# Kernel optimization log

Hardware: AMD Instinct MI355X
Metric: run time of the kernel (lower is better)

The kernel has to match this reference:

```python
import jax, jax.numpy as jnp
import numpy as np

B, N, C, H, PD, CLN = 8, 1024, 512, 8, 256, 64
HD = C // H
HID = 4 * C
LN_EPS = 1e-5
ATT_EPS = 1e-6


def layernorm(x, g, b):
    mu = x.mean(-1, keepdims=True)
    var = ((x - mu) ** 2).mean(-1, keepdims=True)
    return (x - mu) * jax.lax.rsqrt(var + LN_EPS) * g + b


def setup_inputs() -> dict:
    key = jax.random.key(0)
    ks = jax.random.split(key, 16)
    p = lambda k, shp, s=0.02: (jax.random.normal(k, shp, dtype=jnp.float32) * s)
    return {
        "x_token": jax.random.normal(ks[0], (B, N, C), dtype=jnp.float32),
        "x_path": jax.random.normal(ks[1], (B, N, PD), dtype=jnp.float32),
        "wq": p(ks[2], (C, C)),
        "wk": p(ks[3], (C, C)),
        "wv": p(ks[4], (C, C)),
        "w_proj": p(ks[5], (C, C)),
        "b_proj": jnp.zeros((C,), jnp.float32),
        "g1": jnp.ones((C,), jnp.float32),
        "b1": jnp.zeros((C,), jnp.float32),
        "g2": jnp.ones((C,), jnp.float32),
        "b2": jnp.zeros((C,), jnp.float32),
        "w1": p(ks[6], (HID, C)),
        "bb1": jnp.zeros((HID,), jnp.float32),
        "w2": p(ks[7], (C, HID)),
        "bb2": jnp.zeros((C,), jnp.float32),
        "idx_cluster": jax.random.randint(ks[8], (B, N), 0, CLN, dtype=jnp.int64 if jax.config.jax_enable_x64 else jnp.int32),
        "cluster_num": CLN,
    }


def reference(x_token, x_path, wq, wk, wv, w_proj, b_proj, g1, b1, g2, b2,
              w1, bb1, w2, bb2, idx_cluster, cluster_num):
    Bn, Nn, Cn = x_token.shape
    scale = (Cn // H) ** -0.5

    # norm1 + attention
    t = layernorm(x_token, g1, b1)
    q = (t @ wq.T).reshape(Bn, Nn, H, HD).transpose(0, 2, 1, 3)  # bhnd
    k = (t @ wk.T).reshape(Bn, Nn, H, HD).transpose(0, 2, 1, 3)
    v = (t @ wv.T).reshape(Bn, Nn, H, HD).transpose(0, 2, 1, 3)

    # scatter-to-(B,cluster,N,C) then sum over clusters == same-cluster mask on QK^T
    scores = jnp.einsum("bhid,bhjd->bhij", q, k) * scale  # (B,H,N,N)
    same = (idx_cluster[:, None, :, None] == idx_cluster[:, None, None, :])  # (B,1,N,N)
    scores = jnp.where(same, scores, jnp.float32(-1e9))

    # custom eps-stabilized exp-softmax (as in the torch code, no max-subtraction)
    e = jnp.exp(scores.astype(jnp.float32))
    attn = (e + ATT_EPS / Nn) / (e.sum(-1, keepdims=True) + ATT_EPS)

    out = jnp.einsum("bhij,bhjd->bhid", attn, v)
    out = out.transpose(0, 2, 1, 3).reshape(Bn, Nn, Cn)
    out = out @ w_proj.T + b_proj

    x = x_token + out  # drop_path is identity in eval

    # MLP block
    h = layernorm(x, g2, b2)
    m = jax.nn.gelu(h @ w1.T + bb1, approximate=False) @ w2.T + bb2
    return x + m
```

## Files before the change

kernel.cpp:

```cpp
#include <hip/hip_runtime.h>

typedef unsigned short u16;
typedef __attribute__((ext_vector_type(4))) float f32x4;
typedef __attribute__((ext_vector_type(8))) short s16x8;
typedef __attribute__((ext_vector_type(4))) unsigned short u16x4;
typedef __attribute__((ext_vector_type(8))) unsigned short u16x8;

__device__ __forceinline__ u16 f2bf(float f) {
    unsigned int u = __builtin_bit_cast(unsigned int, f);
    u += 0x7fffu + ((u >> 16) & 1u);
    return (u16)(u >> 16);
}
__device__ __forceinline__ float bf2f(u16 h) {
    unsigned int u = ((unsigned int)h) << 16;
    return __builtin_bit_cast(float, u);
}
__device__ __forceinline__ void gload16(const u16* g, u16* l) {
    __builtin_amdgcn_global_load_lds(
        (const __attribute__((address_space(1))) void*)g,
        (__attribute__((address_space(3))) void*)l, 16, 0, 0);
}

__global__ __launch_bounds__(256) void cvt_all(const float* __restrict__ wq,
                                               const float* __restrict__ wk,
                                               const float* __restrict__ wv,
                                               const float* __restrict__ wp,
                                               const float* __restrict__ w1,
                                               const float* __restrict__ w2,
                                               u16* __restrict__ dqkv,
                                               u16* __restrict__ dp,
                                               u16* __restrict__ dw1,
                                               u16* __restrict__ dw2,
                                               float* __restrict__ vsum) {
    int b = blockIdx.x;
    if (b >= 3072) {
        float4 z = {0.f, 0.f, 0.f, 0.f};
        ((float4*)vsum)[(b - 3072) * 256 + threadIdx.x] = z;
        return;
    }
    const float* src; u16* dst; int off;
    if      (b < 256)  { src = wq; dst = dqkv;          off = b; }
    else if (b < 512)  { src = wk; dst = dqkv + 262144; off = b - 256; }
    else if (b < 768)  { src = wv; dst = dqkv + 524288; off = b - 512; }
    else if (b < 1024) { src = wp; dst = dp;            off = b - 768; }
    else if (b < 2048) { src = w1; dst = dw1;           off = b - 1024; }
    else               { src = w2; dst = dw2;           off = b - 2048; }
    int i = off * 256 + threadIdx.x;
    float4 v = ((const float4*)src)[i];
    u16x4 o;
    o.x = f2bf(v.x); o.y = f2bf(v.y); o.z = f2bf(v.z); o.w = f2bf(v.w);
    ((u16x4*)dst)[i] = o;
}

__global__ __launch_bounds__(128) void ln_kernel(const float* __restrict__ in,
                                                 const float* __restrict__ g,
                                                 const float* __restrict__ bta,
                                                 u16* __restrict__ out) {
    int row = blockIdx.x;
    int t = threadIdx.x;
    float4 v = ((const float4*)(in + (size_t)row * 512))[t];
    float s  = v.x + v.y + v.z + v.w;
    float s2 = v.x * v.x + v.y * v.y + v.z * v.z + v.w * v.w;
#pragma unroll
    for (int m = 1; m < 64; m <<= 1) { s += __shfl_xor(s, m); s2 += __shfl_xor(s2, m); }
    __shared__ float sh[4];
    if ((t & 63) == 0) { sh[(t >> 6) * 2] = s; sh[(t >> 6) * 2 + 1] = s2; }
    __syncthreads();
    s = sh[0] + sh[2]; s2 = sh[1] + sh[3];
    float mu  = s * (1.0f / 512.0f);
    float var = s2 * (1.0f / 512.0f) - mu * mu;
    float rstd = rsqrtf(var + 1e-5f);
    float4 gv = ((const float4*)g)[t];
    float4 bv = ((const float4*)bta)[t];
    u16x4 o;
    o.x = f2bf((v.x - mu) * rstd * gv.x + bv.x);
    o.y = f2bf((v.y - mu) * rstd * gv.y + bv.y);
    o.z = f2bf((v.z - mu) * rstd * gv.z + bv.z);
    o.w = f2bf((v.w - mu) * rstd * gv.w + bv.w);
    ((u16x4*)(out + (size_t)row * 512))[t] = o;
}

__global__ __launch_bounds__(512) void vsum_part(const u16* __restrict__ qkv,
                                                 float* __restrict__ vsum) {
    int b = blockIdx.x >> 3, chunk = blockIdx.x & 7;
    int c = threadIdx.x;
    const u16* base = qkv + (size_t)b * 1024 * 1536 + 1024 + c;
    float s = 0.0f;
    for (int n = chunk * 128; n < chunk * 128 + 128; ++n) s += bf2f(base[(size_t)n * 1536]);
    atomicAdd(&vsum[b * 512 + c], s);
}

__global__ __launch_bounds__(1024) void cluster_sort(const int* __restrict__ idx,
                                                     int* __restrict__ perm,
                                                     int* __restrict__ cstart,
                                                     int* __restrict__ ccnt) {
    const int b = blockIdx.x, t = threadIdx.x;
    const int w = t >> 6, lane = t & 63;
    __shared__ int whist[16][64];
    __shared__ int cnt[64];
    __shared__ int off[64];
    ((int*)whist)[t] = 0;
    __syncthreads();
    const int myc = idx[b * 1024 + t];
    atomicAdd(&whist[w][myc], 1);
    int rank_w = 0;
    for (int c = 0; c < 64; ++c) {
        unsigned long long m = __ballot(myc == c);
        if (myc == c) rank_w = __popcll(m & ((1ull << lane) - 1ull));
    }
    __syncthreads();
    if (t < 64) {
        int s = 0;
        for (int ww = 0; ww < 16; ++ww) s += whist[ww][t];
        cnt[t] = s;
        ccnt[b * 64 + t] = s;
    }
    __syncthreads();
    if (t == 0) {
        int s = 0;
        for (int c = 0; c < 64; ++c) { off[c] = s; s += cnt[c]; }
    }
    __syncthreads();
    int cross = 0;
    for (int ww = 0; ww < w; ++ww) cross += whist[ww][myc];
    perm[b * 1024 + off[myc] + cross + rank_w] = t;
    if (t < 64) cstart[b * 64 + t] = off[t];
}

__global__ __launch_bounds__(64) void cattn_kernel(const u16* __restrict__ qkv,
                                                   const int* __restrict__ perm,
                                                   const int* __restrict__ cstart,
                                                   const int* __restrict__ ccnt,
                                                   const float* __restrict__ vsum,
                                                   u16* __restrict__ O) {
    const int bid = blockIdx.x;
    const int h = bid & 7, c = (bid >> 3) & 63, b = bid >> 9;
    const int m = ccnt[b * 64 + c];
    if (m == 0) return;
    const int start = b * 1024 + cstart[b * 64 + c];
    const int lane = threadIdx.x;
    const int fr = lane & 15, fkb = lane >> 4;
    __shared__ __align__(16) u16 Qs[16 * 72];
    __shared__ __align__(16) u16 Ks[32 * 72];
    __shared__ __align__(16) u16 Vt[64 * 36];
    __shared__ __align__(16) u16 Pl[16 * 40];

    const u16* qkv_b = qkv + (size_t)b * 1024 * 1536;
    const float epsN = 1e-6f / 1024.0f;

    for (int q0 = 0; q0 < m; q0 += 16) {
        __syncthreads();
        {
            int row = lane >> 3, seg = lane & 7;
#pragma unroll
            for (int p = 0; p < 2; ++p) {
                int r = row + p * 8;
                int gr = perm[start + min(q0 + r, m - 1)];
                *(int4*)(&Qs[r * 72 + seg * 8]) =
                    *(const int4*)(qkv_b + (size_t)gr * 1536 + h * 64 + seg * 8);
            }
        }
        __syncthreads();
        const s16x8 qf0 = *(const s16x8*)(&Qs[fr * 72 + fkb * 8]);
        const s16x8 qf1 = *(const s16x8*)(&Qs[fr * 72 + 32 + fkb * 8]);

        f32x4 oacc[4] = {};
        float rs[4] = {0.f, 0.f, 0.f, 0.f};

        for (int k0 = 0; k0 < m; k0 += 32) {
            __syncthreads();
            {
                int row = lane >> 3, seg = lane & 7;
#pragma unroll
                for (int p = 0; p < 4; ++p) {
                    int r = row + p * 8;
                    int gr = perm[start + min(k0 + r, m - 1)];
                    const u16* src = qkv_b + (size_t)gr * 1536 + h * 64 + seg * 8;
                    *(int4*)(&Ks[r * 72 + seg * 8]) = *(const int4*)(src + 512);
                    u16x8 vv = *(const u16x8*)(src + 1024);
#pragma unroll
                    for (int i = 0; i < 8; ++i) Vt[(seg * 8 + i) * 36 + r] = vv[i];
                }
            }
            __syncthreads();
#pragma unroll
            for (int ct = 0; ct < 2; ++ct) {
                f32x4 sacc = {};
                s16x8 kf0 = *(const s16x8*)(&Ks[(ct * 16 + fr) * 72 + fkb * 8]);
                s16x8 kf1 = *(const s16x8*)(&Ks[(ct * 16 + fr) * 72 + 32 + fkb * 8]);
                sacc = __builtin_amdgcn_mfma_f32_16x16x32_bf16(qf0, kf0, sacc, 0, 0, 0);
                sacc = __builtin_amdgcn_mfma_f32_16x16x32_bf16(qf1, kf1, sacc, 0, 0, 0);
                bool valid = (k0 + ct * 16 + fr) < m;
#pragma unroll
                for (int r = 0; r < 4; ++r) {
                    float e = valid ? __expf(sacc[r] * 0.125f) : 0.0f;
                    rs[r] += e;
                    Pl[(fkb * 4 + r) * 40 + ct * 16 + fr] = f2bf(e);
                }
            }
            __syncthreads();
            s16x8 pf = *(const s16x8*)(&Pl[fr * 40 + fkb * 8]);
#pragma unroll
            for (int dt = 0; dt < 4; ++dt) {
                s16x8 vf = *(const s16x8*)(&Vt[(dt * 16 + fr) * 36 + fkb * 8]);
                oacc[dt] = __builtin_amdgcn_mfma_f32_16x16x32_bf16(pf, vf, oacc[dt], 0, 0, 0);
            }
        }
#pragma unroll
        for (int r = 0; r < 4; ++r)
#pragma unroll
            for (int mm = 1; mm < 16; mm <<= 1) rs[r] += __shfl_xor(rs[r], mm);

#pragma unroll
        for (int r = 0; r < 4; ++r) {
            int ql = q0 + fkb * 4 + r;
            if (ql < m) {
                int orow = perm[start + ql];
#pragma unroll
                for (int dt = 0; dt < 4; ++dt) {
                    int dcol = dt * 16 + fr;
                    float vs = vsum[(b * 8 + h) * 64 + dcol];
                    float val = (oacc[dt][r] + epsN * vs) / (rs[r] + 1e-6f);
                    O[((size_t)(b * 1024 + orow)) * 512 + h * 64 + dcol] = f2bf(val);
                }
            }
        }
    }
}

template <int BM, int BN, bool OUT_BF16, bool BIAS, bool RESID, bool GELU>
__global__ __launch_bounds__(256) void gemm_sb(const u16* __restrict__ A,
                                               const u16* __restrict__ W,
                                               const float* __restrict__ bias,
                                               const float* __restrict__ resid,
                                               void* __restrict__ outp,
                                               int M, int N, int K) {
    constexpr int MI = BM / 32;
    constexpr int NI = BN / 32;
    __shared__ __align__(16) u16 As[BM * 64];
    __shared__ __align__(16) u16 Bs[BN * 64];
    const int bm = blockIdx.x, bn = blockIdx.y;
    const int t = threadIdx.x;
    const int lane = t & 63, w = t >> 6;
    const int wm = w >> 1, wn = w & 1;
    const int fr = lane & 15, fkb = lane >> 4;
    const int l8 = lane >> 3;
    const int c8s = (((lane & 7) ^ (l8 & 7)) * 8);
    f32x4 acc[MI][NI] = {};
    const u16* Ab = A + (size_t)bm * BM * K;
    const u16* Wb = W + (size_t)bn * BN * K;

    for (int k0 = 0; k0 < K; k0 += 64) {
        __syncthreads();
#pragma unroll
        for (int j = 0; j < MI; ++j) {
            int r = (w * MI + j) * 8 + l8;
            gload16(Ab + (size_t)r * K + k0 + c8s, &As[(w * MI + j) * 512]);
        }
#pragma unroll
        for (int j = 0; j < NI; ++j) {
            int r = (w * NI + j) * 8 + l8;
            gload16(Wb + (size_t)r * K + k0 + c8s, &Bs[(w * NI + j) * 512]);
        }
        __syncthreads();
#pragma unroll
        for (int kk = 0; kk < 64; kk += 32) {
            const int co = (((kk >> 3) + fkb) ^ (fr & 7)) << 3;
            s16x8 af[MI], bfv[NI];
#pragma unroll
            for (int mi = 0; mi < MI; ++mi)
                af[mi] = *(const s16x8*)(&As[(wm * (BM / 2) + mi * 16 + fr) * 64 + co]);
#pragma unroll
            for (int ni = 0; ni < NI; ++ni)
                bfv[ni] = *(const s16x8*)(&Bs[(wn * (BN / 2) + ni * 16 + fr) * 64 + co]);
#pragma unroll
            for (int mi = 0; mi < MI; ++mi)
#pragma unroll
                for (int ni = 0; ni < NI; ++ni)
                    acc[mi][ni] = __builtin_amdgcn_mfma_f32_16x16x32_bf16(
                        af[mi], bfv[ni], acc[mi][ni], 0, 0, 0);
        }
    }

    const int rg = (lane >> 4) * 4;
#pragma unroll
    for (int mi = 0; mi < MI; ++mi) {
#pragma unroll
        for (int ni = 0; ni < NI; ++ni) {
            int gcol = bn * BN + wn * (BN / 2) + ni * 16 + fr;
            float bv = BIAS ? bias[gcol] : 0.0f;
#pragma unroll
            for (int r = 0; r < 4; ++r) {
                int grow = bm * BM + wm * (BM / 2) + mi * 16 + rg + r;
                float v = acc[mi][ni][r] + bv;
                if (GELU) v = 0.5f * v * (1.0f + erff(v * 0.70710678118f));
                if (RESID) v += resid[(size_t)grow * N + gcol];
                if (OUT_BF16)
                    ((u16*)outp)[(size_t)grow * N + gcol] = f2bf(v);
                else
                    ((float*)outp)[(size_t)grow * N + gcol] = v;
            }
        }
    }
}

extern "C" void kernel_launch(void* const* d_in, const int* in_sizes, int n_in,
                              void* d_out, int out_size, void* d_ws, size_t ws_size,
                              hipStream_t stream) {
    const float* x_token = (const float*)d_in[0];
    const float* wq     = (const float*)d_in[2];
    const float* wk     = (const float*)d_in[3];
    const float* wv     = (const float*)d_in[4];
    const float* w_proj = (const float*)d_in[5];
    const float* b_proj = (const float*)d_in[6];
    const float* g1     = (const float*)d_in[7];
    const float* b1     = (const float*)d_in[8];
    const float* g2     = (const float*)d_in[9];
    const float* b2     = (const float*)d_in[10];
    const float* w1     = (const float*)d_in[11];
    const float* bb1    = (const float*)d_in[12];
    const float* w2     = (const float*)d_in[13];
    const float* bb2    = (const float*)d_in[14];
    const int*   idx    = (const int*)d_in[15];
    float* out_f = (float*)d_out;

    char* ws = (char*)d_ws;
    u16*   t_buf = (u16*)(ws);
    u16*   qkv   = (u16*)(ws + 8388608);
    u16*   Obuf  = (u16*)(ws + 8388608 + 25165824);
    u16*   m1    = qkv;
    float* xbuf  = (float*)(ws + 41943040);
    u16*   h_buf = t_buf;
    char*  wsw   = ws + 58720256;
    u16*   wqkv  = (u16*)(wsw);
    u16*   wprjb = (u16*)(wsw + 1572864);
    u16*   w1b   = (u16*)(wsw + 2097152);
    u16*   w2b   = (u16*)(wsw + 4194304);
    float* vsum  = (float*)(wsw + 6291456);
    int*   perm   = (int*)xbuf;
    int*   cstart = (int*)((char*)xbuf + 32768);
    int*   ccnt   = (int*)((char*)xbuf + 34816);
    (void)ws_size; (void)in_sizes; (void)n_in; (void)out_size;

    cvt_all<<<3076, 256, 0, stream>>>(wq, wk, wv, w_proj, w1, w2,
                                      wqkv, wprjb, w1b, w2b, vsum);
    cluster_sort<<<8, 1024, 0, stream>>>(idx, perm, cstart, ccnt);

    ln_kernel<<<8192, 128, 0, stream>>>(x_token, g1, b1, t_buf);
    gemm_sb<64, 128, true, false, false, false><<<dim3(128, 12), 256, 0, stream>>>(
        t_buf, wqkv, nullptr, nullptr, qkv, 8192, 1536, 512);
    vsum_part<<<64, 512, 0, stream>>>(qkv, vsum);
    cattn_kernel<<<4096, 64, 0, stream>>>(qkv, perm, cstart, ccnt, vsum, Obuf);
    gemm_sb<64, 64, false, true, true, false><<<dim3(128, 8), 256, 0, stream>>>(
        Obuf, wprjb, b_proj, x_token, xbuf, 8192, 512, 512);
    ln_kernel<<<8192, 128, 0, stream>>>(xbuf, g2, b2, h_buf);
    gemm_sb<64, 128, true, true, false, true><<<dim3(128, 16), 256, 0, stream>>>(
        h_buf, w1b, bb1, nullptr, m1, 8192, 2048, 512);
    gemm_sb<64, 64, false, true, true, false><<<dim3(128, 8), 256, 0, stream>>>(
        m1, w2b, bb2, xbuf, out_f, 8192, 512, 2048);
}
```

Measured before the change: 148.6 us.

## Fuse V column-sum into QKV GEMM epilogue and store residual x in bf16

Removes the separate vsum_part kernel by reducing V-column sums from the QKV GEMM accumulators, using shuffles and then atomics into vsum. It also stores the intermediate residual x in bf16 instead of fp32, which halves the traffic for the LN2 read and the final residual read. The vsum now comes from the fp32 accumulators rather than the rounded bf16 values, and keeping the residual in bf16 loses precision in the skip connection.

```diff
diff --git a/kernel.cpp b/kernel.cpp
--- a/kernel.cpp
+++ b/kernel.cpp
@@ -52,13 +52,20 @@
     ((u16x4*)dst)[i] = o;
 }
 
-__global__ __launch_bounds__(128) void ln_kernel(const float* __restrict__ in,
+template <bool IN_BF16>
+__global__ __launch_bounds__(128) void ln_kernel(const void* __restrict__ inp,
                                                  const float* __restrict__ g,
                                                  const float* __restrict__ bta,
                                                  u16* __restrict__ out) {
     int row = blockIdx.x;
     int t = threadIdx.x;
-    float4 v = ((const float4*)(in + (size_t)row * 512))[t];
+    float4 v;
+    if (IN_BF16) {
+        u16x4 hv = ((const u16x4*)inp)[row * 128 + t];
+        v.x = bf2f(hv.x); v.y = bf2f(hv.y); v.z = bf2f(hv.z); v.w = bf2f(hv.w);
+    } else {
+        v = ((const float4*)inp)[row * 128 + t];
+    }
     float s  = v.x + v.y + v.z + v.w;
     float s2 = v.x * v.x + v.y * v.y + v.z * v.z + v.w * v.w;
 #pragma unroll
@@ -78,16 +85,6 @@
     o.z = f2bf((v.z - mu) * rstd * gv.z + bv.z);
     o.w = f2bf((v.w - mu) * rstd * gv.w + bv.w);
     ((u16x4*)(out + (size_t)row * 512))[t] = o;
-}
-
-__global__ __launch_bounds__(512) void vsum_part(const u16* __restrict__ qkv,
-                                                 float* __restrict__ vsum) {
-    int b = blockIdx.x >> 3, chunk = blockIdx.x & 7;
-    int c = threadIdx.x;
-    const u16* base = qkv + (size_t)b * 1024 * 1536 + 1024 + c;
-    float s = 0.0f;
-    for (int n = chunk * 128; n < chunk * 128 + 128; ++n) s += bf2f(base[(size_t)n * 1536]);
-    atomicAdd(&vsum[b * 512 + c], s);
 }
 
 __global__ __launch_bounds__(1024) void cluster_sort(const int* __restrict__ idx,
@@ -228,12 +225,13 @@
     }
 }
 
-template <int BM, int BN, bool OUT_BF16, bool BIAS, bool RESID, bool GELU>
+template <int BM, int BN, bool OUT_BF16, bool BIAS, int RESID, bool GELU, bool VSUM>
 __global__ __launch_bounds__(256) void gemm_sb(const u16* __restrict__ A,
                                                const u16* __restrict__ W,
                                                const float* __restrict__ bias,
-                                               const float* __restrict__ resid,
+                                               const void* __restrict__ resid,
                                                void* __restrict__ outp,
+                                               float* __restrict__ vsum,
                                                int M, int N, int K) {
     constexpr int MI = BM / 32;
     constexpr int NI = BN / 32;
@@ -294,11 +292,30 @@
                 int grow = bm * BM + wm * (BM / 2) + mi * 16 + rg + r;
                 float v = acc[mi][ni][r] + bv;
                 if (GELU) v = 0.5f * v * (1.0f + erff(v * 0.70710678118f));
-                if (RESID) v += resid[(size_t)grow * N + gcol];
+                if (RESID == 1) v += ((const float*)resid)[(size_t)grow * N + gcol];
+                if (RESID == 2) v += bf2f(((const u16*)resid)[(size_t)grow * N + gcol]);
                 if (OUT_BF16)
                     ((u16*)outp)[(size_t)grow * N + gcol] = f2bf(v);
                 else
                     ((float*)outp)[(size_t)grow * N + gcol] = v;
+            }
+        }
+    }
+
+    if (VSUM && bn * BN >= 1024) {
+        const int vb = (bm * BM) >> 10;
+#pragma unroll
+        for (int ni = 0; ni < NI; ++ni) {
+            float p = 0.0f;
+#pragma unroll
+            for (int mi = 0; mi < MI; ++mi)
+#pragma unroll
+                for (int r = 0; r < 4; ++r) p += acc[mi][ni][r];
+            p += __shfl_xor(p, 16);
+            p += __shfl_xor(p, 32);
+            if (lane < 16) {
+                int gcol = bn * BN + wn * (BN / 2) + ni * 16 + lane;
+                atomicAdd(&vsum[vb * 512 + gcol - 1024], p);
             }
         }
     }
@@ -329,7 +346,7 @@
     u16*   qkv   = (u16*)(ws + 8388608);
     u16*   Obuf  = (u16*)(ws + 8388608 + 25165824);
     u16*   m1    = qkv;
-    float* xbuf  = (float*)(ws + 41943040);
+    u16*   x_bf  = (u16*)(ws + 41943040);
     u16*   h_buf = t_buf;
     char*  wsw   = ws + 58720256;
     u16*   wqkv  = (u16*)(wsw);
@@ -337,25 +354,24 @@
     u16*   w1b   = (u16*)(wsw + 2097152);
     u16*   w2b   = (u16*)(wsw + 4194304);
     float* vsum  = (float*)(wsw + 6291456);
-    int*   perm   = (int*)xbuf;
-    int*   cstart = (int*)((char*)xbuf + 32768);
-    int*   ccnt   = (int*)((char*)xbuf + 34816);
+    int*   perm   = (int*)(ws + 41943040);
+    int*   cstart = (int*)(ws + 41943040 + 32768);
+    int*   ccnt   = (int*)(ws + 41943040 + 34816);
     (void)ws_size; (void)in_sizes; (void)n_in; (void)out_size;
 
     cvt_all<<<3076, 256, 0, stream>>>(wq, wk, wv, w_proj, w1, w2,
                                       wqkv, wprjb, w1b, w2b, vsum);
     cluster_sort<<<8, 1024, 0, stream>>>(idx, perm, cstart, ccnt);
 
-    ln_kernel<<<8192, 128, 0, stream>>>(x_token, g1, b1, t_buf);
-    gemm_sb<64, 128, true, false, false, false><<<dim3(128, 12), 256, 0, stream>>>(
-        t_buf, wqkv, nullptr, nullptr, qkv, 8192, 1536, 512);
-    vsum_part<<<64, 512, 0, stream>>>(qkv, vsum);
+    ln_kernel<false><<<8192, 128, 0, stream>>>(x_token, g1, b1, t_buf);
+    gemm_sb<64, 128, true, false, 0, false, true><<<dim3(128, 12), 256, 0, stream>>>(
+        t_buf, wqkv, nullptr, nullptr, qkv, vsum, 8192, 1536, 512);
     cattn_kernel<<<4096, 64, 0, stream>>>(qkv, perm, cstart, ccnt, vsum, Obuf);
-    gemm_sb<64, 64, false, true, true, false><<<dim3(128, 8), 256, 0, stream>>>(
-        Obuf, wprjb, b_proj, x_token, xbuf, 8192, 512, 512);
-    ln_kernel<<<8192, 128, 0, stream>>>(xbuf, g2, b2, h_buf);
-    gemm_sb<64, 128, true, true, false, true><<<dim3(128, 16), 256, 0, stream>>>(
-        h_buf, w1b, bb1, nullptr, m1, 8192, 2048, 512);
-    gemm_sb<64, 64, false, true, true, false><<<dim3(128, 8), 256, 0, stream>>>(
-        m1, w2b, bb2, xbuf, out_f, 8192, 512, 2048);
-}
+    gemm_sb<64, 64, true, true, 1, false, false><<<dim3(128, 8), 256, 0, stream>>>(
+        Obuf, wprjb, b_proj, x_token, x_bf, nullptr, 8192, 512, 512);
+    ln_kernel<true><<<8192, 128, 0, stream>>>(x_bf, g2, b2, h_buf);
+    gemm_sb<64, 128, true, true, 0, true, false><<<dim3(128, 16), 256, 0, stream>>>(
+        h_buf, w1b, bb1, nullptr, m1, nullptr, 8192, 2048, 512);
+    gemm_sb<64, 64, false, true, 2, false, false><<<dim3(128, 8), 256, 0, stream>>>(
+        m1, w2b, bb2, x_bf, out_f, nullptr, 8192, 512, 2048);
+}
```

Result: faster. 132.8 us (-10.6%).
